# Kernel tuning notes

Measured on AMD Instinct MI355X. Metric: run time of the kernel, lower is better.

Reference implementation:

```python
import jax, jax.numpy as jnp
import numpy as np

C = 256          # channels
K_SIZE = 3       # involution kernel size
GROUPS = 16      # groups g
HIDDEN = C // 4  # reduction_ratio = 4
B, H, W = 8, 64, 64


def setup_inputs() -> dict:
    key = jax.random.key(0)
    k0, k1, k2 = jax.random.split(key, 3)
    kk = K_SIZE * K_SIZE
    return {
        "x": jax.random.normal(k0, (B, C, H, W), dtype=jnp.float32),
        # 1x1 conv weights stored as matrices [out_ch, in_ch]
        "w_reduce": jax.random.normal(k1, (HIDDEN, C), dtype=jnp.float32) * 0.05,
        "b_reduce": jnp.zeros((HIDDEN,), dtype=jnp.float32),
        "w_span": jax.random.normal(k2, (GROUPS * kk, HIDDEN), dtype=jnp.float32) * 0.05,
        "b_span": jnp.zeros((GROUPS * kk,), dtype=jnp.float32),
    }


def reference(x, w_reduce, b_reduce, w_span, b_span):
    b, c, h, w = x.shape
    k, g = K_SIZE, GROUPS
    kk = k * k
    # stride == 1 -> sigma is identity; kernel generator: 1x1 conv -> relu -> 1x1 conv
    hid = jax.nn.relu(jnp.einsum('oc,bcxy->boxy', w_reduce, x)
                      + b_reduce[None, :, None, None])
    Kmap = (jnp.einsum('oc,bcxy->boxy', w_span, hid)
            + b_span[None, :, None, None])            # [B, g*kk, H, W]
    Kmap = Kmap.reshape(b, g, kk, h, w)
    # unfold with padding k//2, stride 1: extract k*k shifted views
    pad = k // 2
    xp = jnp.pad(x, ((0, 0), (0, 0), (pad, pad), (pad, pad)))
    patches = jnp.stack(
        [xp[:, :, i:i + h, j:j + w] for i in range(k) for j in range(k)],
        axis=2)                                        # [B, C, kk, H, W]
    patches = patches.reshape(b, g, c // g, kk, h, w)
    # location-specific, channel-agnostic multiply-reduce over kk
    out = jnp.einsum('bgnkhw,bgkhw->bgnhw', patches, Kmap)
    return out.reshape(b, c, h, w)
```

## Files before the change

kernel.cpp:

```cpp
#include <hip/hip_runtime.h>

#define CCH   256
#define HIDN  64
#define GK    144
#define NB    8
#define NHW   4096

#define W1T_OFF  0
#define W2T_OFF  16384

__global__ __launch_bounds__(256) void wtrans_kernel(
    const float* __restrict__ w_reduce, const float* __restrict__ w_span,
    float* __restrict__ ws)
{
    const int idx = blockIdx.x * 256 + threadIdx.x;
    if (idx < 16384) {
        const int c = idx >> 6, o = idx & 63;
        ws[W1T_OFF + idx] = w_reduce[o * CCH + c];
    } else {
        const int i2 = idx - 16384;
        const int o = i2 / 144, j = i2 - o * 144;
        ws[W2T_OFF + i2] = w_span[j * HIDN + o];
    }
}

__global__ __launch_bounds__(512, 4) void invol_fused(
    const float* __restrict__ x,
    const float* __restrict__ b_reduce,
    const float* __restrict__ b_span,
    const float* __restrict__ ws_ro,
    float* __restrict__ out)
{
    __shared__ float smem[16384];
    float (*xs)[64] = (float (*)[64])smem;

    const float* __restrict__ w1T = ws_ro + W1T_OFF;
    const float* __restrict__ w2T = ws_ro + W2T_OFF;

    const int lane = threadIdx.x & 63;
    const int wid  = __builtin_amdgcn_readfirstlane(threadIdx.x >> 6);

    const int raw = blockIdx.x;
    const int row = ((raw & 7) << 6) | (raw >> 3);
    const int b   = row >> 6;
    const int hr  = row & 63;

    const float* xb = x + (size_t)b * (CCH * NHW) + hr * 64;

    {
        const int cl = lane >> 4;
        const int p4 = (lane & 15) * 4;
        #pragma unroll
        for (int t = 0; t < 8; ++t) {
            const int c0 = wid * 32 + t * 4;
            const float* src = xb + (size_t)(c0 + cl) * NHW + p4;
            __builtin_amdgcn_global_load_lds(
                (const __attribute__((address_space(1))) unsigned int*)src,
                (__attribute__((address_space(3))) unsigned int*)&xs[c0][0],
                16, 0, 0);
        }
    }
    __syncthreads();

    const int o0 = wid * 8;
    float acc[8];
    #pragma unroll
    for (int i = 0; i < 8; ++i) acc[i] = b_reduce[o0 + i];

    #pragma unroll 8
    for (int c = 0; c < CCH; ++c) {
        const float xv = xs[c][lane];
        const float* w1c = w1T + c * HIDN + o0;
        #pragma unroll
        for (int i = 0; i < 8; ++i)
            acc[i] = fmaf(w1c[i], xv, acc[i]);
    }
    __syncthreads();

    float (*hid)[64] = (float (*)[64])smem;
    #pragma unroll
    for (int i = 0; i < 8; ++i) hid[o0 + i][lane] = fmaxf(acc[i], 0.0f);
    __syncthreads();

    const int j0 = wid * 18;
    float kv[18];
    #pragma unroll
    for (int jj = 0; jj < 18; ++jj) kv[jj] = b_span[j0 + jj];

    #pragma unroll 4
    for (int o = 0; o < HIDN; ++o) {
        const float hv = hid[o][lane];
        const float* w2o = w2T + o * GK + j0;
        #pragma unroll
        for (int jj = 0; jj < 18; ++jj)
            kv[jj] = fmaf(w2o[jj], hv, kv[jj]);
    }

    const bool vwm = (lane > 0), vwp = (lane < 63);
    const bool vhm = (hr  > 0), vhp = (hr  < 63);
    const bool vk[9] = { vhm && vwm, vhm, vhm && vwp,
                         vwm,        true, vwp,
                         vhp && vwm, vhp, vhp && vwp };
    #pragma unroll
    for (int jj = 0; jj < 18; ++jj)
        kv[jj] = vk[jj % 9] ? kv[jj] : 0.0f;

    const int oWm = vwm ? -1  : 0, oWp = vwp ? 1  : 0;
    const int oHm = vhm ? -64 : 0, oHp = vhp ? 64 : 0;
    const int oo[9] = { oHm + oWm, oHm, oHm + oWp,
                        oWm,       0,   oWp,
                        oHp + oWm, oHp, oHp + oWp };

    const float* xrow = xb + lane;
    float*       orow = out + (size_t)b * (CCH * NHW) + hr * 64 + lane;

    #pragma unroll 4
    for (int m = 0; m < 32; ++m) {
        const int c  = wid * 32 + m;
        const int gl = m >> 4;
        const float* xc = xrow + (size_t)c * NHW;
        float a = 0.0f;
        #pragma unroll
        for (int k = 0; k < 9; ++k)
            a = fmaf(xc[oo[k]], kv[gl * 9 + k], a);
        orow[(size_t)c * NHW] = a;
    }
}

extern "C" void kernel_launch(void* const* d_in, const int* in_sizes, int n_in,
                              void* d_out, int out_size, void* d_ws, size_t ws_size,
                              hipStream_t stream) {
    const float* x        = (const float*)d_in[0];
    const float* w_reduce = (const float*)d_in[1];
    const float* b_reduce = (const float*)d_in[2];
    const float* w_span   = (const float*)d_in[3];
    const float* b_span   = (const float*)d_in[4];
    float* out = (float*)d_out;
    float* ws  = (float*)d_ws;

    wtrans_kernel<<<dim3(100), dim3(256), 0, stream>>>(w_reduce, w_span, ws);
    invol_fused<<<dim3(NB * 64), dim3(512), 0, stream>>>(
        x, b_reduce, b_span, ws, out);
}
```

Baseline: 121.4 us.

## Remap reduce GEMM so lanes own hidden channels and stage span weights in LDS

The first 1x1 conv is remapped so each lane owns one hidden channel and each wave owns 8 pixels. Weights arrive as per-lane float4 loads from a reorganized transposed layout, and x values come as LDS broadcast float4 reads. Previously every lane issued scalar loads of the same weights from global memory. The hidden activations are now written to a padded (stride 65) LDS buffer, transposed so the second conv can read them back per pixel. The span weights are also copied into LDS with padding so they can be read as vectors. The aim is to replace redundant global weight traffic with vectorized LDS accesses, at the cost of extra LDS staging and possible bank conflicts.

```diff
diff --git a/kernel.cpp b/kernel.cpp
--- a/kernel.cpp
+++ b/kernel.cpp
@@ -15,8 +15,8 @@
 {
     const int idx = blockIdx.x * 256 + threadIdx.x;
     if (idx < 16384) {
-        const int c = idx >> 6, o = idx & 63;
-        ws[W1T_OFF + idx] = w_reduce[o * CCH + c];
+        const int cc = idx & 3, o = (idx >> 2) & 63, c4 = idx >> 8;
+        ws[W1T_OFF + idx] = w_reduce[o * CCH + c4 * 4 + cc];
     } else {
         const int i2 = idx - 16384;
         const int o = i2 / 144, j = i2 - o * 144;
@@ -31,14 +31,14 @@
     const float* __restrict__ ws_ro,
     float* __restrict__ out)
 {
-    __shared__ float smem[16384];
+    __shared__ __align__(16) float smem[16384];
     float (*xs)[64] = (float (*)[64])smem;
-
-    const float* __restrict__ w1T = ws_ro + W1T_OFF;
-    const float* __restrict__ w2T = ws_ro + W2T_OFF;
+    float* const w2s = smem;
+    float* const hid = smem + 10240;
 
     const int lane = threadIdx.x & 63;
     const int wid  = __builtin_amdgcn_readfirstlane(threadIdx.x >> 6);
+    const int tid  = threadIdx.x;
 
     const int raw = blockIdx.x;
     const int row = ((raw & 7) << 6) | (raw >> 3);
@@ -62,24 +62,48 @@
     }
     __syncthreads();
 
-    const int o0 = wid * 8;
+    const int p8 = wid * 8;
+    const float4* w1p = (const float4*)(ws_ro + W1T_OFF);
     float acc[8];
-    #pragma unroll
-    for (int i = 0; i < 8; ++i) acc[i] = b_reduce[o0 + i];
+    {
+        const float bias = b_reduce[lane];
+        #pragma unroll
+        for (int p = 0; p < 8; ++p) acc[p] = bias;
+    }
 
-    #pragma unroll 8
-    for (int c = 0; c < CCH; ++c) {
-        const float xv = xs[c][lane];
-        const float* w1c = w1T + c * HIDN + o0;
+    #pragma unroll 4
+    for (int c4 = 0; c4 < 64; ++c4) {
+        const float4 wv = w1p[c4 * 64 + lane];
         #pragma unroll
-        for (int i = 0; i < 8; ++i)
-            acc[i] = fmaf(w1c[i], xv, acc[i]);
+        for (int cc = 0; cc < 4; ++cc) {
+            const int c = c4 * 4 + cc;
+            const float4 x0 = *(const float4*)&xs[c][p8];
+            const float4 x1 = *(const float4*)&xs[c][p8 + 4];
+            const float wcc = (cc == 0) ? wv.x : (cc == 1) ? wv.y
+                            : (cc == 2) ? wv.z : wv.w;
+            acc[0] = fmaf(wcc, x0.x, acc[0]);
+            acc[1] = fmaf(wcc, x0.y, acc[1]);
+            acc[2] = fmaf(wcc, x0.z, acc[2]);
+            acc[3] = fmaf(wcc, x0.w, acc[3]);
+            acc[4] = fmaf(wcc, x1.x, acc[4]);
+            acc[5] = fmaf(wcc, x1.y, acc[5]);
+            acc[6] = fmaf(wcc, x1.z, acc[6]);
+            acc[7] = fmaf(wcc, x1.w, acc[7]);
+        }
     }
     __syncthreads();
 
-    float (*hid)[64] = (float (*)[64])smem;
     #pragma unroll
-    for (int i = 0; i < 8; ++i) hid[o0 + i][lane] = fmaxf(acc[i], 0.0f);
+    for (int p = 0; p < 8; ++p)
+        hid[(p8 + p) * 65 + lane] = fmaxf(acc[p], 0.0f);
+
+    {
+        const int o2 = tid >> 3, w8 = tid & 7;
+        const float2* src = (const float2*)(ws_ro + W2T_OFF + o2 * 144 + w8 * 18);
+        float2* dst = (float2*)(w2s + o2 * 160 + w8 * 20);
+        #pragma unroll
+        for (int r = 0; r < 9; ++r) dst[r] = src[r];
+    }
     __syncthreads();
 
     const int j0 = wid * 18;
@@ -87,13 +111,21 @@
     #pragma unroll
     for (int jj = 0; jj < 18; ++jj) kv[jj] = b_span[j0 + jj];
 
-    #pragma unroll 4
+    #pragma unroll 2
     for (int o = 0; o < HIDN; ++o) {
-        const float hv = hid[o][lane];
-        const float* w2o = w2T + o * GK + j0;
-        #pragma unroll
-        for (int jj = 0; jj < 18; ++jj)
-            kv[jj] = fmaf(w2o[jj], hv, kv[jj]);
+        const float hv = hid[lane * 65 + o];
+        const float4* wp = (const float4*)(w2s + o * 160 + wid * 20);
+        const float4 wa = wp[0], wb = wp[1], wc = wp[2], wd = wp[3];
+        const float2 we = *(const float2*)(w2s + o * 160 + wid * 20 + 16);
+        kv[ 0] = fmaf(wa.x, hv, kv[ 0]);  kv[ 1] = fmaf(wa.y, hv, kv[ 1]);
+        kv[ 2] = fmaf(wa.z, hv, kv[ 2]);  kv[ 3] = fmaf(wa.w, hv, kv[ 3]);
+        kv[ 4] = fmaf(wb.x, hv, kv[ 4]);  kv[ 5] = fmaf(wb.y, hv, kv[ 5]);
+        kv[ 6] = fmaf(wb.z, hv, kv[ 6]);  kv[ 7] = fmaf(wb.w, hv, kv[ 7]);
+        kv[ 8] = fmaf(wc.x, hv, kv[ 8]);  kv[ 9] = fmaf(wc.y, hv, kv[ 9]);
+        kv[10] = fmaf(wc.z, hv, kv[10]);  kv[11] = fmaf(wc.w, hv, kv[11]);
+        kv[12] = fmaf(wd.x, hv, kv[12]);  kv[13] = fmaf(wd.y, hv, kv[13]);
+        kv[14] = fmaf(wd.z, hv, kv[14]);  kv[15] = fmaf(wd.w, hv, kv[15]);
+        kv[16] = fmaf(we.x, hv, kv[16]);  kv[17] = fmaf(we.y, hv, kv[17]);
     }
 
     const bool vwm = (lane > 0), vwp = (lane < 63);
```

New measurement: 125.8 us. 1.04x slower.

## Compute kernel-generator 1x1 convs with bf16 MFMA and split-precision weights

Applied to the files above, without the earlier changes.

Both 1x1 convolutions of the kernel generator move from scalar FMA loops onto MFMA 16x16x32 bf16 instructions. The weights are prepacked into MFMA fragment layout as hi/lo bf16 pairs to keep extra precision, and activations are converted to bf16 into padded LDS. The generated kernel map is staged through LDS in bf16 before the final 3x3 involution, and the occupancy hint is raised from 4 to 6. This cuts FMA work and weight reloads but loses precision on x, hidden and Kmap values, which could exceed tolerance.

```diff
diff --git a/kernel.cpp b/kernel.cpp
--- a/kernel.cpp
+++ b/kernel.cpp
@@ -1,44 +1,77 @@
 #include <hip/hip_runtime.h>
 
-#define CCH   256
-#define HIDN  64
-#define GK    144
-#define NB    8
-#define NHW   4096
-
-#define W1T_OFF  0
-#define W2T_OFF  16384
-
-__global__ __launch_bounds__(256) void wtrans_kernel(
+#define CCH 256
+#define HIDN 64
+#define NB  8
+#define NHW 4096
+
+#define W1PK_OFF 0
+#define W2PK_OFF 16384
+
+typedef __attribute__((ext_vector_type(8))) short bf16x8;
+typedef __attribute__((ext_vector_type(4))) float f32x4;
+typedef __attribute__((ext_vector_type(4))) int   i32x4;
+typedef __attribute__((ext_vector_type(2))) int   i32x2;
+
+__device__ __forceinline__ unsigned short bf16_rne(float f) {
+    unsigned u = __float_as_uint(f);
+    u += 0x7FFFu + ((u >> 16) & 1u);
+    return (unsigned short)(u >> 16);
+}
+__device__ __forceinline__ float bf16_f32(unsigned short s) {
+    return __uint_as_float(((unsigned)s) << 16);
+}
+__device__ __forceinline__ bf16x8 as_bf16(i32x4 v) {
+    union { i32x4 i; bf16x8 b; } u; u.i = v; return u.b;
+}
+
+__global__ __launch_bounds__(256) void prepack_kernel(
     const float* __restrict__ w_reduce, const float* __restrict__ w_span,
-    float* __restrict__ ws)
+    unsigned* __restrict__ ws)
 {
     const int idx = blockIdx.x * 256 + threadIdx.x;
+    int d, lane, pass, ks, mt, K, base;
+    const float* W;
     if (idx < 16384) {
-        const int c = idx >> 6, o = idx & 63;
-        ws[W1T_OFF + idx] = w_reduce[o * CCH + c];
+        d = idx & 3; lane = (idx >> 2) & 63; pass = (idx >> 8) & 1;
+        ks = (idx >> 9) & 7; mt = (idx >> 12) & 3;
+        W = w_reduce; K = 256; base = W1PK_OFF + idx;
     } else {
         const int i2 = idx - 16384;
-        const int o = i2 / 144, j = i2 - o * 144;
-        ws[W2T_OFF + i2] = w_span[j * HIDN + o];
-    }
-}
-
-__global__ __launch_bounds__(512, 4) void invol_fused(
+        d = i2 & 3; lane = (i2 >> 2) & 63; pass = (i2 >> 8) & 1;
+        ks = (i2 >> 9) & 1; mt = i2 >> 10;
+        W = w_span; K = 64; base = W2PK_OFF + i2;
+    }
+    const int m = mt * 16 + (lane & 15);
+    const int g = (lane >> 4) & 3;
+    unsigned o = 0;
+    #pragma unroll
+    for (int h = 0; h < 2; ++h) {
+        const int ei = d * 2 + h;
+        const int k  = ks * 32 + ((ei >> 2) << 4) + (g << 2) + (ei & 3);
+        const float w = W[m * K + k];
+        const unsigned short hi = bf16_rne(w);
+        const unsigned short v  = pass ? bf16_rne(w - bf16_f32(hi)) : hi;
+        o |= ((unsigned)v) << (16 * h);
+    }
+    ws[base] = o;
+}
+
+__global__ __launch_bounds__(512, 6) void invol_fused(
     const float* __restrict__ x,
     const float* __restrict__ b_reduce,
     const float* __restrict__ b_span,
-    const float* __restrict__ ws_ro,
+    const unsigned* __restrict__ wpk,
     float* __restrict__ out)
 {
-    __shared__ float smem[16384];
-    float (*xs)[64] = (float (*)[64])smem;
-
-    const float* __restrict__ w1T = ws_ro + W1T_OFF;
-    const float* __restrict__ w2T = ws_ro + W2T_OFF;
-
-    const int lane = threadIdx.x & 63;
-    const int wid  = __builtin_amdgcn_readfirstlane(threadIdx.x >> 6);
+    __shared__ __align__(16) int lds[8576];
+    short* const lds_s = (short*)lds;
+
+    const int tid  = threadIdx.x;
+    const int lane = tid & 63;
+    const int wid  = __builtin_amdgcn_readfirstlane(tid >> 6);
+    const int n    = lane & 15;
+    const int g    = lane >> 4;
 
     const int raw = blockIdx.x;
     const int row = ((raw & 7) << 6) | (raw >> 3);
@@ -48,63 +81,104 @@
     const float* xb = x + (size_t)b * (CCH * NHW) + hr * 64;
 
     {
-        const int cl = lane >> 4;
-        const int p4 = (lane & 15) * 4;
+        const int px = tid & 63;
+        const int c0 = (tid >> 6) * 32;
+        const float* xp = xb + (size_t)c0 * NHW + px;
+        int* dst = &lds[px * 134 + (c0 >> 1)];
         #pragma unroll
-        for (int t = 0; t < 8; ++t) {
-            const int c0 = wid * 32 + t * 4;
-            const float* src = xb + (size_t)(c0 + cl) * NHW + p4;
-            __builtin_amdgcn_global_load_lds(
-                (const __attribute__((address_space(1))) unsigned int*)src,
-                (__attribute__((address_space(3))) unsigned int*)&xs[c0][0],
-                16, 0, 0);
+        for (int i = 0; i < 16; ++i) {
+            const float f0 = xp[(2 * i) * NHW];
+            const float f1 = xp[(2 * i + 1) * NHW];
+            dst[i] = (int)((unsigned)bf16_rne(f0) |
+                           ((unsigned)bf16_rne(f1) << 16));
         }
     }
     __syncthreads();
 
-    const int o0 = wid * 8;
-    float acc[8];
+    const int ot  = wid >> 1;
+    const int pt0 = (wid & 1) * 2;
+    f32x4 acc0 = {0.f, 0.f, 0.f, 0.f};
+    f32x4 acc1 = {0.f, 0.f, 0.f, 0.f};
+    const int* w1pk = (const int*)wpk + W1PK_OFF;
+
     #pragma unroll
-    for (int i = 0; i < 8; ++i) acc[i] = b_reduce[o0 + i];
-
-    #pragma unroll 8
-    for (int c = 0; c < CCH; ++c) {
-        const float xv = xs[c][lane];
-        const float* w1c = w1T + c * HIDN + o0;
+    for (int ks = 0; ks < 8; ++ks) {
+        const int abase = ot * 4096 + ks * 512 + lane * 4;
+        const i32x4 ah = *(const i32x4*)(w1pk + abase);
+        const i32x4 al = *(const i32x4*)(w1pk + abase + 256);
+        const int bb0 = (pt0 * 16 + n) * 134 + ks * 16 + g * 2;
+        const int bb1 = bb0 + 16 * 134;
+        const i32x2 p0 = *(const i32x2*)&lds[bb0];
+        const i32x2 p1 = *(const i32x2*)&lds[bb0 + 8];
+        const i32x2 q0 = *(const i32x2*)&lds[bb1];
+        const i32x2 q1 = *(const i32x2*)&lds[bb1 + 8];
+        const i32x4 b0 = {p0.x, p0.y, p1.x, p1.y};
+        const i32x4 b1 = {q0.x, q0.y, q1.x, q1.y};
+        const bf16x8 fa_h = as_bf16(ah), fa_l = as_bf16(al);
+        const bf16x8 fb0 = as_bf16(b0), fb1 = as_bf16(b1);
+        acc0 = __builtin_amdgcn_mfma_f32_16x16x32_bf16(fa_h, fb0, acc0, 0, 0, 0);
+        acc0 = __builtin_amdgcn_mfma_f32_16x16x32_bf16(fa_l, fb0, acc0, 0, 0, 0);
+        acc1 = __builtin_amdgcn_mfma_f32_16x16x32_bf16(fa_h, fb1, acc1, 0, 0, 0);
+        acc1 = __builtin_amdgcn_mfma_f32_16x16x32_bf16(fa_l, fb1, acc1, 0, 0, 0);
+    }
+    __syncthreads();
+
+    {
+        const f32x4 br = *(const f32x4*)&b_reduce[ot * 16 + g * 4];
+        const unsigned h00 = (unsigned)bf16_rne(fmaxf(acc0.x + br.x, 0.f))
+                           | ((unsigned)bf16_rne(fmaxf(acc0.y + br.y, 0.f)) << 16);
+        const unsigned h01 = (unsigned)bf16_rne(fmaxf(acc0.z + br.z, 0.f))
+                           | ((unsigned)bf16_rne(fmaxf(acc0.w + br.w, 0.f)) << 16);
+        const unsigned h10 = (unsigned)bf16_rne(fmaxf(acc1.x + br.x, 0.f))
+                           | ((unsigned)bf16_rne(fmaxf(acc1.y + br.y, 0.f)) << 16);
+        const unsigned h11 = (unsigned)bf16_rne(fmaxf(acc1.z + br.z, 0.f))
+                           | ((unsigned)bf16_rne(fmaxf(acc1.w + br.w, 0.f)) << 16);
+        const i32x2 w0 = {(int)h00, (int)h01};
+        const i32x2 w1 = {(int)h10, (int)h11};
+        *(i32x2*)&lds[(pt0 * 16 + n) * 38 + ot * 8 + g * 2]       = w0;
+        *(i32x2*)&lds[((pt0 + 1) * 16 + n) * 38 + ot * 8 + g * 2] = w1;
+    }
+    __syncthreads();
+
+    const int* w2pk = (const int*)wpk + W2PK_OFF;
+    for (int t = wid; t < 36; t += 8) {
+        const int jt = t >> 2, pt = t & 3;
+        f32x4 acc = {0.f, 0.f, 0.f, 0.f};
         #pragma unroll
-        for (int i = 0; i < 8; ++i)
-            acc[i] = fmaf(w1c[i], xv, acc[i]);
-    }
-    __syncthreads();
-
-    float (*hid)[64] = (float (*)[64])smem;
-    #pragma unroll
-    for (int i = 0; i < 8; ++i) hid[o0 + i][lane] = fmaxf(acc[i], 0.0f);
-    __syncthreads();
-
-    const int j0 = wid * 18;
-    float kv[18];
-    #pragma unroll
-    for (int jj = 0; jj < 18; ++jj) kv[jj] = b_span[j0 + jj];
-
-    #pragma unroll 4
-    for (int o = 0; o < HIDN; ++o) {
-        const float hv = hid[o][lane];
-        const float* w2o = w2T + o * GK + j0;
-        #pragma unroll
-        for (int jj = 0; jj < 18; ++jj)
-            kv[jj] = fmaf(w2o[jj], hv, kv[jj]);
-    }
+        for (int ks = 0; ks < 2; ++ks) {
+            const int abase = jt * 1024 + ks * 512 + lane * 4;
+            const i32x4 ah = *(const i32x4*)(w2pk + abase);
+            const i32x4 al = *(const i32x4*)(w2pk + abase + 256);
+            const int bb = (pt * 16 + n) * 38 + ks * 16 + g * 2;
+            const i32x2 p0 = *(const i32x2*)&lds[bb];
+            const i32x2 p1 = *(const i32x2*)&lds[bb + 8];
+            const i32x4 bi = {p0.x, p0.y, p1.x, p1.y};
+            const bf16x8 fb = as_bf16(bi);
+            acc = __builtin_amdgcn_mfma_f32_16x16x32_bf16(as_bf16(ah), fb, acc, 0, 0, 0);
+            acc = __builtin_amdgcn_mfma_f32_16x16x32_bf16(as_bf16(al), fb, acc, 0, 0, 0);
+        }
+        const f32x4 bs = *(const f32x4*)&b_span[jt * 16 + g * 4];
+        const int jb = jt * 16 + g * 4;
+        const int pxi = pt * 16 + n;
+        lds_s[4864 + (jb + 0) * 66 + pxi] = (short)bf16_rne(acc.x + bs.x);
+        lds_s[4864 + (jb + 1) * 66 + pxi] = (short)bf16_rne(acc.y + bs.y);
+        lds_s[4864 + (jb + 2) * 66 + pxi] = (short)bf16_rne(acc.z + bs.z);
+        lds_s[4864 + (jb + 3) * 66 + pxi] = (short)bf16_rne(acc.w + bs.w);
+    }
+    __syncthreads();
 
     const bool vwm = (lane > 0), vwp = (lane < 63);
     const bool vhm = (hr  > 0), vhp = (hr  < 63);
     const bool vk[9] = { vhm && vwm, vhm, vhm && vwp,
                          vwm,        true, vwp,
                          vhp && vwm, vhp, vhp && vwp };
+    float kv[18];
     #pragma unroll
-    for (int jj = 0; jj < 18; ++jj)
-        kv[jj] = vk[jj % 9] ? kv[jj] : 0.0f;
-
+    for (int jj = 0; jj < 18; ++jj) {
+        const float v = bf16_f32((unsigned short)
+                        lds_s[4864 + (wid * 18 + jj) * 66 + lane]);
+        kv[jj] = vk[jj % 9] ? v : 0.f;
+    }
     const int oWm = vwm ? -1  : 0, oWp = vwp ? 1  : 0;
     const int oHm = vhm ? -64 : 0, oHp = vhp ? 64 : 0;
     const int oo[9] = { oHm + oWm, oHm, oHm + oWp,
@@ -119,7 +193,7 @@
         const int c  = wid * 32 + m;
         const int gl = m >> 4;
         const float* xc = xrow + (size_t)c * NHW;
-        float a = 0.0f;
+        float a = 0.f;
         #pragma unroll
         for (int k = 0; k < 9; ++k)
             a = fmaf(xc[oo[k]], kv[gl * 9 + k], a);
@@ -136,9 +210,9 @@
     const float* w_span   = (const float*)d_in[3];
     const float* b_span   = (const float*)d_in[4];
     float* out = (float*)d_out;
-    float* ws  = (float*)d_ws;
-
-    wtrans_kernel<<<dim3(100), dim3(256), 0, stream>>>(w_reduce, w_span, ws);
+    unsigned* ws = (unsigned*)d_ws;
+
+    prepack_kernel<<<dim3(100), dim3(256), 0, stream>>>(w_reduce, w_span, ws);
     invol_fused<<<dim3(NB * 64), dim3(512), 0, stream>>>(
         x, b_reduce, b_span, ws, out);
 }
```

New measurement: 130.3 us. 7.3% more time.
